# Kernel optimization log

Hardware: AMD Instinct MI355X
Metric: run time of the kernel (lower is better)

## Reference

```python
import jax, jax.numpy as jnp
import numpy as np

N_NODES = 100000
N_EDGES = 1600000
D_IN = 128
D_OUT = 128


def setup_inputs() -> dict:
    key = jax.random.key(0)
    k1, k2, k3, k4, k5, k6 = jax.random.split(key, 6)
    x = jax.random.normal(k1, (N_NODES, D_IN), dtype=jnp.float32)
    adj_rows = jnp.sort(jax.random.randint(k2, (N_EDGES,), 0, N_NODES, dtype=jnp.int32))
    adj_cols = jax.random.randint(k3, (N_EDGES,), 0, N_NODES, dtype=jnp.int32)
    adj_vals = jax.random.uniform(k4, (N_EDGES,), dtype=jnp.float32)
    weight = jax.random.normal(k5, (D_OUT, D_IN), dtype=jnp.float32) * (1.0 / np.sqrt(D_IN))
    bias = jax.random.normal(k6, (D_OUT,), dtype=jnp.float32) * 0.01
    return {"x": x, "adj_rows": adj_rows, "adj_cols": adj_cols,
            "adj_vals": adj_vals, "weight": weight, "bias": bias}


def reference(x, adj_rows, adj_cols, adj_vals, weight, bias):
    # w_input = inputs @ W.T  -> [N, D_OUT]
    w_input = x @ weight.T
    # SpMM: out[r] = sum_e adj_vals[e] * w_input[cols[e]] for edges with rows[e] == r
    msgs = adj_vals[:, None] * w_input[adj_cols]          # [E, D_OUT]
    agg = jax.ops.segment_sum(msgs, adj_rows, num_segments=N_NODES)
    out = jax.nn.relu(agg + bias)
    return out.astype(jnp.float32)
```

## Files before the change

kernel.cpp:

```cpp
#include <hip/hip_runtime.h>
#include <hip/hip_bf16.h>

#define D 128
#define RPW 8

typedef __attribute__((ext_vector_type(8))) short bf16x8;
typedef __attribute__((ext_vector_type(4))) float f32x4;

__device__ __forceinline__ unsigned short f2bf(float f) {
    union { float f; unsigned u; } uf{f};
    unsigned r = uf.u + 0x7fffu + ((uf.u >> 16) & 1u);
    return (unsigned short)(r >> 16);
}
__device__ __forceinline__ unsigned pack2(float a, float b) {
    return (unsigned)f2bf(a) | ((unsigned)f2bf(b) << 16);
}
__device__ __forceinline__ float bflo(unsigned u) {
    union { unsigned u; float f; } c{u << 16};
    return c.f;
}
__device__ __forceinline__ float bfhi(unsigned u) {
    union { unsigned u; float f; } c{u & 0xffff0000u};
    return c.f;
}

#define FMA8(A, vv, u) \
    A[0] = fmaf(vv, bflo(u.x), A[0]); A[1] = fmaf(vv, bfhi(u.x), A[1]); \
    A[2] = fmaf(vv, bflo(u.y), A[2]); A[3] = fmaf(vv, bfhi(u.y), A[3]); \
    A[4] = fmaf(vv, bflo(u.z), A[4]); A[5] = fmaf(vv, bfhi(u.z), A[5]); \
    A[6] = fmaf(vv, bflo(u.w), A[6]); A[7] = fmaf(vv, bfhi(u.w), A[7]);

__global__ __launch_bounds__(256) void build_rowptr(const int* __restrict__ rows,
                                                    const float* __restrict__ W,
                                                    unsigned short* __restrict__ wbf,
                                                    int2* __restrict__ rowptr,
                                                    int e, int n) {
    int i = blockIdx.x * 256 + threadIdx.x;
    if (i < D * D) wbf[i] = f2bf(W[i]);
    if (i >= e) return;
    int r = rows[i];
    int prev = (i == 0) ? -1 : rows[i - 1];
    int next = (i == e - 1) ? n : rows[i + 1];
    if (prev != r) {
        rowptr[r].x = i;
        for (int q = prev + 1; q < r; ++q) rowptr[q] = make_int2(i, i);
    }
    if (next != r) {
        rowptr[r].y = i + 1;
        if (i == e - 1)
            for (int q = r + 1; q < n; ++q) rowptr[q] = make_int2(e, e);
    }
}

__global__ __launch_bounds__(256) void gemm_mfma(const float* __restrict__ x,
                                                 const unsigned short* __restrict__ wbf,
                                                 unsigned short* __restrict__ wi,
                                                 int nrows) {
    const int lane = threadIdx.x & 63;
    const int row0 = blockIdx.x * 128 + (threadIdx.x >> 6) * 32;
    const int lrow = lane & 15;
    const int lk8 = (lane >> 4) * 8;

    bf16x8 afrag[2][4];
#pragma unroll
    for (int rb = 0; rb < 2; ++rb)
#pragma unroll
        for (int kb = 0; kb < 4; ++kb) {
            int gr = min(row0 + rb * 16 + lrow, nrows - 1);
            const float4* p = (const float4*)(x + (size_t)gr * D + kb * 32 + lk8);
            float4 f0 = p[0], f1 = p[1];
            union { bf16x8 v; unsigned u[4]; } cv;
            cv.u[0] = pack2(f0.x, f0.y);
            cv.u[1] = pack2(f0.z, f0.w);
            cv.u[2] = pack2(f1.x, f1.y);
            cv.u[3] = pack2(f1.z, f1.w);
            afrag[rb][kb] = cv.v;
        }

    f32x4 acc[2][8];
#pragma unroll
    for (int rb = 0; rb < 2; ++rb)
#pragma unroll
        for (int nb = 0; nb < 8; ++nb)
            acc[rb][nb] = (f32x4){0.f, 0.f, 0.f, 0.f};

#pragma unroll
    for (int nb = 0; nb < 8; ++nb) {
#pragma unroll
        for (int kb = 0; kb < 4; ++kb) {
            bf16x8 bfrag = *(const bf16x8*)(wbf + (nb * 16 + lrow) * 128 + kb * 32 + lk8);
            acc[0][nb] = __builtin_amdgcn_mfma_f32_16x16x32_bf16(afrag[0][kb], bfrag, acc[0][nb], 0, 0, 0);
            acc[1][nb] = __builtin_amdgcn_mfma_f32_16x16x32_bf16(afrag[1][kb], bfrag, acc[1][nb], 0, 0, 0);
        }
    }

#pragma unroll
    for (int rb = 0; rb < 2; ++rb)
#pragma unroll
        for (int j = 0; j < 4; ++j) {
            int gr = row0 + rb * 16 + (lane >> 4) * 4 + j;
            if (gr < nrows) {
#pragma unroll
                for (int nb = 0; nb < 8; ++nb)
                    wi[(size_t)gr * D + nb * 16 + lrow] = f2bf(acc[rb][nb][j]);
            }
        }
}

__global__ __launch_bounds__(256) void spmm_relu(const unsigned short* __restrict__ wi,
                                                 const int2* __restrict__ rowptr,
                                                 const int* __restrict__ cols,
                                                 const float* __restrict__ vals,
                                                 const float* __restrict__ bias,
                                                 float* __restrict__ out,
                                                 int n) {
    const int lane = threadIdx.x & 63;
    const int R0 = (blockIdx.x * 4 + (threadIdx.x >> 6)) * RPW;
    if (R0 >= n) return;
    const int nr = min(RPW, n - R0);

    const int2 rp = rowptr[R0 + min(lane, nr - 1)];
    const int ch = (lane & 15) * 8;
    const int sub = lane >> 4;

    float4 b0 = *(const float4*)(bias + (lane & 15) * 8);
    float4 b1 = *(const float4*)(bias + (lane & 15) * 8 + 4);

    int s = __shfl(rp.x, 0), e = __shfl(rp.y, 0);
    int c = 0; float v = 0.f;
    { int idx = s + lane; if (idx < e) { c = cols[idx]; v = vals[idx]; } }

    for (int j = 0; j < nr; ++j) {
        int s_n = 0, e_n = 0, c_n = 0; float v_n = 0.f;
        if (j + 1 < nr) {
            s_n = __shfl(rp.x, j + 1); e_n = __shfl(rp.y, j + 1);
            int idx = s_n + lane; if (idx < e_n) { c_n = cols[idx]; v_n = vals[idx]; }
        }

        float a0[8] = {0.f, 0.f, 0.f, 0.f, 0.f, 0.f, 0.f, 0.f};
        float a1[8] = {0.f, 0.f, 0.f, 0.f, 0.f, 0.f, 0.f, 0.f};

        const int cnt = min(e - s, 64);
        for (int q = 0; q * 4 < cnt; q += 4) {
            const int i0 = q * 4 + sub;
            int   c0 = __shfl(c, i0),     c1 = __shfl(c, i0 + 4);
            int   c2 = __shfl(c, i0 + 8), c3 = __shfl(c, i0 + 12);
            float v0 = __shfl(v, i0),     v1 = __shfl(v, i0 + 4);
            float v2 = __shfl(v, i0 + 8), v3 = __shfl(v, i0 + 12);
            uint4 u0 = *(const uint4*)(wi + (size_t)c0 * D + ch);
            uint4 u1 = *(const uint4*)(wi + (size_t)c1 * D + ch);
            uint4 u2 = *(const uint4*)(wi + (size_t)c2 * D + ch);
            uint4 u3 = *(const uint4*)(wi + (size_t)c3 * D + ch);
            FMA8(a0, v0, u0); FMA8(a1, v1, u1);
            FMA8(a0, v2, u2); FMA8(a1, v3, u3);
        }
        for (int base = s + 64; base < e; base += 64) {
            int cc = 0; float vv = 0.f;
            { int idx = base + lane; if (idx < e) { cc = cols[idx]; vv = vals[idx]; } }
            const int cnt2 = min(e - base, 64);
            for (int q = 0; q * 4 < cnt2; q += 4) {
                const int i0 = q * 4 + sub;
                int   c0 = __shfl(cc, i0),     c1 = __shfl(cc, i0 + 4);
                int   c2 = __shfl(cc, i0 + 8), c3 = __shfl(cc, i0 + 12);
                float v0 = __shfl(vv, i0),     v1 = __shfl(vv, i0 + 4);
                float v2 = __shfl(vv, i0 + 8), v3 = __shfl(vv, i0 + 12);
                uint4 u0 = *(const uint4*)(wi + (size_t)c0 * D + ch);
                uint4 u1 = *(const uint4*)(wi + (size_t)c1 * D + ch);
                uint4 u2 = *(const uint4*)(wi + (size_t)c2 * D + ch);
                uint4 u3 = *(const uint4*)(wi + (size_t)c3 * D + ch);
                FMA8(a0, v0, u0); FMA8(a1, v1, u1);
                FMA8(a0, v2, u2); FMA8(a1, v3, u3);
            }
        }

        float r8[8];
#pragma unroll
        for (int t = 0; t < 8; ++t) {
            float sjj = a0[t] + a1[t];
            sjj += __shfl_xor(sjj, 16);
            sjj += __shfl_xor(sjj, 32);
            r8[t] = sjj;
        }
        if (lane < 16) {
            float4 o0, o1;
            o0.x = fmaxf(r8[0] + b0.x, 0.f);
            o0.y = fmaxf(r8[1] + b0.y, 0.f);
            o0.z = fmaxf(r8[2] + b0.z, 0.f);
            o0.w = fmaxf(r8[3] + b0.w, 0.f);
            o1.x = fmaxf(r8[4] + b1.x, 0.f);
            o1.y = fmaxf(r8[5] + b1.y, 0.f);
            o1.z = fmaxf(r8[6] + b1.z, 0.f);
            o1.w = fmaxf(r8[7] + b1.w, 0.f);
            *(float4*)(out + (size_t)(R0 + j) * D + lane * 8) = o0;
            *(float4*)(out + (size_t)(R0 + j) * D + lane * 8 + 4) = o1;
        }

        s = s_n; e = e_n; c = c_n; v = v_n;
    }
}

extern "C" void kernel_launch(void* const* d_in, const int* in_sizes, int n_in,
                              void* d_out, int out_size, void* d_ws, size_t ws_size,
                              hipStream_t stream) {
    const float* x        = (const float*)d_in[0];
    const int*   adj_rows = (const int*)d_in[1];
    const int*   adj_cols = (const int*)d_in[2];
    const float* adj_vals = (const float*)d_in[3];
    const float* weight   = (const float*)d_in[4];
    const float* bias     = (const float*)d_in[5];
    float*       out      = (float*)d_out;

    const int n = in_sizes[0] / D;
    const int e = in_sizes[1];

    unsigned short* wi = (unsigned short*)d_ws;
    size_t off = ((size_t)n * D * sizeof(unsigned short) + 255) & ~(size_t)255;
    int2* rowptr = (int2*)((char*)d_ws + off);
    unsigned short* wbf = (unsigned short*)(rowptr + n);

    build_rowptr<<<(e + 255) / 256, 256, 0, stream>>>(adj_rows, weight, wbf,
                                                      rowptr, e, n);

    gemm_mfma<<<(n + 127) / 128, 256, 0, stream>>>(x, wbf, wi, n);

    const int rows_per_block = 4 * RPW;
    spmm_relu<<<(n + rows_per_block - 1) / rows_per_block, 256, 0, stream>>>(
        wi, rowptr, adj_cols, adj_vals, bias, out, n);
}
```

Baseline: 100.9 us.

## Process two rows per wave in SpMM and vectorize GEMM output stores

```diff
diff --git a/kernel.cpp b/kernel.cpp
--- a/kernel.cpp
+++ b/kernel.cpp
@@ -2,7 +2,6 @@
 #include <hip/hip_bf16.h>
 
 #define D 128
-#define RPW 8
 
 typedef __attribute__((ext_vector_type(8))) short bf16x8;
 typedef __attribute__((ext_vector_type(4))) float f32x4;
@@ -61,12 +60,12 @@
     const int lrow = lane & 15;
     const int lk8 = (lane >> 4) * 8;
 
-    bf16x8 afrag[2][4];
-#pragma unroll
-    for (int rb = 0; rb < 2; ++rb)
+    bf16x8 xfrag[2][4];
+#pragma unroll
+    for (int xb = 0; xb < 2; ++xb)
 #pragma unroll
         for (int kb = 0; kb < 4; ++kb) {
-            int gr = min(row0 + rb * 16 + lrow, nrows - 1);
+            int gr = min(row0 + xb * 16 + lrow, nrows - 1);
             const float4* p = (const float4*)(x + (size_t)gr * D + kb * 32 + lk8);
             float4 f0 = p[0], f1 = p[1];
             union { bf16x8 v; unsigned u[4]; } cv;
@@ -74,37 +73,39 @@
             cv.u[1] = pack2(f0.z, f0.w);
             cv.u[2] = pack2(f1.x, f1.y);
             cv.u[3] = pack2(f1.z, f1.w);
-            afrag[rb][kb] = cv.v;
+            xfrag[xb][kb] = cv.v;
         }
 
     f32x4 acc[2][8];
 #pragma unroll
-    for (int rb = 0; rb < 2; ++rb)
-#pragma unroll
-        for (int nb = 0; nb < 8; ++nb)
-            acc[rb][nb] = (f32x4){0.f, 0.f, 0.f, 0.f};
-
-#pragma unroll
-    for (int nb = 0; nb < 8; ++nb) {
+    for (int xb = 0; xb < 2; ++xb)
+#pragma unroll
+        for (int cb = 0; cb < 8; ++cb)
+            acc[xb][cb] = (f32x4){0.f, 0.f, 0.f, 0.f};
+
+#pragma unroll
+    for (int cb = 0; cb < 8; ++cb) {
 #pragma unroll
         for (int kb = 0; kb < 4; ++kb) {
-            bf16x8 bfrag = *(const bf16x8*)(wbf + (nb * 16 + lrow) * 128 + kb * 32 + lk8);
-            acc[0][nb] = __builtin_amdgcn_mfma_f32_16x16x32_bf16(afrag[0][kb], bfrag, acc[0][nb], 0, 0, 0);
-            acc[1][nb] = __builtin_amdgcn_mfma_f32_16x16x32_bf16(afrag[1][kb], bfrag, acc[1][nb], 0, 0, 0);
-        }
-    }
-
-#pragma unroll
-    for (int rb = 0; rb < 2; ++rb)
-#pragma unroll
-        for (int j = 0; j < 4; ++j) {
-            int gr = row0 + rb * 16 + (lane >> 4) * 4 + j;
-            if (gr < nrows) {
-#pragma unroll
-                for (int nb = 0; nb < 8; ++nb)
-                    wi[(size_t)gr * D + nb * 16 + lrow] = f2bf(acc[rb][nb][j]);
+            bf16x8 wfrag = *(const bf16x8*)(wbf + (cb * 16 + lrow) * 128 + kb * 32 + lk8);
+            acc[0][cb] = __builtin_amdgcn_mfma_f32_16x16x32_bf16(wfrag, xfrag[0][kb], acc[0][cb], 0, 0, 0);
+            acc[1][cb] = __builtin_amdgcn_mfma_f32_16x16x32_bf16(wfrag, xfrag[1][kb], acc[1][cb], 0, 0, 0);
+        }
+    }
+
+#pragma unroll
+    for (int xb = 0; xb < 2; ++xb) {
+        int g = row0 + xb * 16 + lrow;
+        if (g < nrows) {
+#pragma unroll
+            for (int cb = 0; cb < 8; ++cb) {
+                uint2 o;
+                o.x = pack2(acc[xb][cb][0], acc[xb][cb][1]);
+                o.y = pack2(acc[xb][cb][2], acc[xb][cb][3]);
+                *(uint2*)(wi + (size_t)g * D + cb * 16 + (lane >> 4) * 4) = o;
             }
         }
+    }
 }
 
 __global__ __launch_bounds__(256) void spmm_relu(const unsigned short* __restrict__ wi,
@@ -115,87 +116,87 @@
                                                  float* __restrict__ out,
                                                  int n) {
     const int lane = threadIdx.x & 63;
-    const int R0 = (blockIdx.x * 4 + (threadIdx.x >> 6)) * RPW;
-    if (R0 >= n) return;
-    const int nr = min(RPW, n - R0);
-
-    const int2 rp = rowptr[R0 + min(lane, nr - 1)];
+    const int w = blockIdx.x * 4 + (threadIdx.x >> 6);
+    const int rA = w * 2;
+    if (rA >= n) return;
+    const bool has2 = (rA + 1 < n);
+
+    int2 rpA, rpB;
+    if (has2) {
+        int4 rp = *(const int4*)(rowptr + rA);
+        rpA = make_int2(rp.x, rp.y);
+        rpB = make_int2(rp.z, rp.w);
+    } else {
+        rpA = rowptr[rA];
+        rpB = make_int2(0, 0);
+    }
+
     const int ch = (lane & 15) * 8;
     const int sub = lane >> 4;
 
-    float4 b0 = *(const float4*)(bias + (lane & 15) * 8);
-    float4 b1 = *(const float4*)(bias + (lane & 15) * 8 + 4);
-
-    int s = __shfl(rp.x, 0), e = __shfl(rp.y, 0);
-    int c = 0; float v = 0.f;
-    { int idx = s + lane; if (idx < e) { c = cols[idx]; v = vals[idx]; } }
-
-    for (int j = 0; j < nr; ++j) {
-        int s_n = 0, e_n = 0, c_n = 0; float v_n = 0.f;
-        if (j + 1 < nr) {
-            s_n = __shfl(rp.x, j + 1); e_n = __shfl(rp.y, j + 1);
-            int idx = s_n + lane; if (idx < e_n) { c_n = cols[idx]; v_n = vals[idx]; }
-        }
-
-        float a0[8] = {0.f, 0.f, 0.f, 0.f, 0.f, 0.f, 0.f, 0.f};
-        float a1[8] = {0.f, 0.f, 0.f, 0.f, 0.f, 0.f, 0.f, 0.f};
-
-        const int cnt = min(e - s, 64);
-        for (int q = 0; q * 4 < cnt; q += 4) {
-            const int i0 = q * 4 + sub;
-            int   c0 = __shfl(c, i0),     c1 = __shfl(c, i0 + 4);
-            int   c2 = __shfl(c, i0 + 8), c3 = __shfl(c, i0 + 12);
-            float v0 = __shfl(v, i0),     v1 = __shfl(v, i0 + 4);
-            float v2 = __shfl(v, i0 + 8), v3 = __shfl(v, i0 + 12);
-            uint4 u0 = *(const uint4*)(wi + (size_t)c0 * D + ch);
-            uint4 u1 = *(const uint4*)(wi + (size_t)c1 * D + ch);
-            uint4 u2 = *(const uint4*)(wi + (size_t)c2 * D + ch);
-            uint4 u3 = *(const uint4*)(wi + (size_t)c3 * D + ch);
-            FMA8(a0, v0, u0); FMA8(a1, v1, u1);
-            FMA8(a0, v2, u2); FMA8(a1, v3, u3);
-        }
-        for (int base = s + 64; base < e; base += 64) {
-            int cc = 0; float vv = 0.f;
-            { int idx = base + lane; if (idx < e) { cc = cols[idx]; vv = vals[idx]; } }
-            const int cnt2 = min(e - base, 64);
-            for (int q = 0; q * 4 < cnt2; q += 4) {
-                const int i0 = q * 4 + sub;
-                int   c0 = __shfl(cc, i0),     c1 = __shfl(cc, i0 + 4);
-                int   c2 = __shfl(cc, i0 + 8), c3 = __shfl(cc, i0 + 12);
-                float v0 = __shfl(vv, i0),     v1 = __shfl(vv, i0 + 4);
-                float v2 = __shfl(vv, i0 + 8), v3 = __shfl(vv, i0 + 12);
-                uint4 u0 = *(const uint4*)(wi + (size_t)c0 * D + ch);
-                uint4 u1 = *(const uint4*)(wi + (size_t)c1 * D + ch);
-                uint4 u2 = *(const uint4*)(wi + (size_t)c2 * D + ch);
-                uint4 u3 = *(const uint4*)(wi + (size_t)c3 * D + ch);
-                FMA8(a0, v0, u0); FMA8(a1, v1, u1);
-                FMA8(a0, v2, u2); FMA8(a1, v3, u3);
-            }
-        }
-
-        float r8[8];
-#pragma unroll
-        for (int t = 0; t < 8; ++t) {
-            float sjj = a0[t] + a1[t];
-            sjj += __shfl_xor(sjj, 16);
-            sjj += __shfl_xor(sjj, 32);
-            r8[t] = sjj;
-        }
-        if (lane < 16) {
-            float4 o0, o1;
-            o0.x = fmaxf(r8[0] + b0.x, 0.f);
-            o0.y = fmaxf(r8[1] + b0.y, 0.f);
-            o0.z = fmaxf(r8[2] + b0.z, 0.f);
-            o0.w = fmaxf(r8[3] + b0.w, 0.f);
-            o1.x = fmaxf(r8[4] + b1.x, 0.f);
-            o1.y = fmaxf(r8[5] + b1.y, 0.f);
-            o1.z = fmaxf(r8[6] + b1.z, 0.f);
-            o1.w = fmaxf(r8[7] + b1.w, 0.f);
-            *(float4*)(out + (size_t)(R0 + j) * D + lane * 8) = o0;
-            *(float4*)(out + (size_t)(R0 + j) * D + lane * 8 + 4) = o1;
-        }
-
-        s = s_n; e = e_n; c = c_n; v = v_n;
+    float a[8] = {0.f, 0.f, 0.f, 0.f, 0.f, 0.f, 0.f, 0.f};
+    float b[8] = {0.f, 0.f, 0.f, 0.f, 0.f, 0.f, 0.f, 0.f};
+
+    int baseA = rpA.x, baseB = rpB.x;
+    const int eA = rpA.y, eB = rpB.y;
+
+    while (baseA < eA || baseB < eB) {
+        int cA[4], cB[4];
+        float vA[4], vB[4];
+#pragma unroll
+        for (int p = 0; p < 4; ++p) {
+            int iA = baseA + p * 4 + sub;
+            int iB = baseB + p * 4 + sub;
+            bool okA = iA < eA, okB = iB < eB;
+            int jA = okA ? iA : 0;
+            int jB = okB ? iB : 0;
+            cA[p] = okA ? cols[jA] : 0;
+            vA[p] = okA ? vals[jA] : 0.f;
+            cB[p] = okB ? cols[jB] : 0;
+            vB[p] = okB ? vals[jB] : 0.f;
+        }
+        uint4 uA[4], uB[4];
+#pragma unroll
+        for (int p = 0; p < 4; ++p) uA[p] = *(const uint4*)(wi + (size_t)cA[p] * D + ch);
+#pragma unroll
+        for (int p = 0; p < 4; ++p) uB[p] = *(const uint4*)(wi + (size_t)cB[p] * D + ch);
+#pragma unroll
+        for (int p = 0; p < 4; ++p) {
+            FMA8(a, vA[p], uA[p]);
+            FMA8(b, vB[p], uB[p]);
+        }
+        baseA += 16;
+        baseB += 16;
+    }
+
+    float r[8];
+#pragma unroll
+    for (int t = 0; t < 8; ++t) {
+        float sA = a[t];
+        sA += __shfl_xor(sA, 16);
+        sA += __shfl_xor(sA, 32);
+        float sB = b[t];
+        sB += __shfl_xor(sB, 16);
+        sB += __shfl_xor(sB, 32);
+        r[t] = (lane < 16) ? sA : sB;
+    }
+
+    const int myrow = rA + (lane >> 4);
+    if (lane < 32 && myrow < n) {
+        const int cb = (lane & 15) * 8;
+        float4 b0 = *(const float4*)(bias + cb);
+        float4 b1 = *(const float4*)(bias + cb + 4);
+        float4 o0, o1;
+        o0.x = fmaxf(r[0] + b0.x, 0.f);
+        o0.y = fmaxf(r[1] + b0.y, 0.f);
+        o0.z = fmaxf(r[2] + b0.z, 0.f);
+        o0.w = fmaxf(r[3] + b0.w, 0.f);
+        o1.x = fmaxf(r[4] + b1.x, 0.f);
+        o1.y = fmaxf(r[5] + b1.y, 0.f);
+        o1.z = fmaxf(r[6] + b1.z, 0.f);
+        o1.w = fmaxf(r[7] + b1.w, 0.f);
+        *(float4*)(out + (size_t)myrow * D + cb) = o0;
+        *(float4*)(out + (size_t)myrow * D + cb + 4) = o1;
     }
 }
 
@@ -223,7 +224,7 @@
 
     gemm_mfma<<<(n + 127) / 128, 256, 0, stream>>>(x, wbf, wi, n);
 
-    const int rows_per_block = 4 * RPW;
-    spmm_relu<<<(n + rows_per_block - 1) / rows_per_block, 256, 0, stream>>>(
-        wi, rowptr, adj_cols, adj_vals, bias, out, n);
-}
+    const int nwaves = (n + 1) / 2;
+    spmm_relu<<<(nwaves + 3) / 4, 256, 0, stream>>>(wi, rowptr, adj_cols, adj_vals,
+                                                    bias, out, n);
+}
```

After: 131.3 us. 1.3x slower.
